# Optimization experiments

Measured on AMD Instinct MI355X. Metric: run time of the kernel, lower is better.

The kernel has to match this reference:

```python
import jax, jax.numpy as jnp
import numpy as np

VOCAB, EMB, UNITS = 2000, 64, 512
B, T = 64, 128

def lstm(x_emb, Wx, Wh, b, h0, c0):
    """Keras LSTM: gates order (i, f, g, o), sigmoid recurrent activation, tanh activation.
    x_emb: [B, T, EMB]. Returns (H [B,T,U], h [B,U], c [B,U])."""
    # Precompute input contribution for all timesteps (one big GEMM)
    xz = jnp.einsum('bte,eu->btu', x_emb, Wx) + b  # [B, T, 4U]

    def step(carry, xz_t):
        h, c = carry
        z = xz_t + h @ Wh  # [B, 4U]
        i, f, g, o = jnp.split(z, 4, axis=-1)
        i = jax.nn.sigmoid(i)
        f = jax.nn.sigmoid(f)
        g = jnp.tanh(g)
        o = jax.nn.sigmoid(o)
        c = f * c + i * g
        h = o * jnp.tanh(c)
        return (h, c), h

    (h, c), H = jax.lax.scan(step, (h0, c0), jnp.swapaxes(xz, 0, 1))
    return jnp.swapaxes(H, 0, 1), h, c


def setup_inputs() -> dict:
    key = jax.random.key(0)
    ks = jax.random.split(key, 10)
    s = 0.05
    return {
        'x': jax.random.randint(ks[0], (B, T), 0, VOCAB),
        'y': jax.random.randint(ks[1], (B, T), 0, VOCAB),
        'enc_emb': jax.random.normal(ks[2], (VOCAB, EMB), jnp.float32) * s,
        'enc_Wx': jax.random.normal(ks[3], (EMB, 4 * UNITS), jnp.float32) * s,
        'enc_Wh': jax.random.normal(ks[4], (UNITS, 4 * UNITS), jnp.float32) * s,
        'enc_b': jnp.zeros((4 * UNITS,), jnp.float32),
        'dec_emb': jax.random.normal(ks[5], (VOCAB, EMB), jnp.float32) * s,
        'dec_Wx': jax.random.normal(ks[6], (EMB, 4 * UNITS), jnp.float32) * s,
        'dec_Wh': jax.random.normal(ks[7], (UNITS, 4 * UNITS), jnp.float32) * s,
        'dec_b': jnp.zeros((4 * UNITS,), jnp.float32),
        'dense_W': jax.random.normal(ks[8], (2 * UNITS, VOCAB), jnp.float32) * s,
        'dense_b': jnp.zeros((VOCAB,), jnp.float32),
    }


def reference(x, y, enc_emb, enc_Wx, enc_Wh, enc_b,
              dec_emb, dec_Wx, dec_Wh, dec_b, dense_W, dense_b):
    z0 = jnp.zeros((x.shape[0], UNITS), jnp.float32)
    # Encoder
    H, h, c = lstm(enc_emb[x], enc_Wx, enc_Wh, enc_b, z0, z0)  # H: [B,T,U]
    # Decoder LSTM
    s0 = h
    S, h2, c2 = lstm(dec_emb[y], dec_Wx, dec_Wh, dec_b, h, c)  # S: [B,T,U]
    # Shifted states as attention queries (teacher forcing, Luong dot-attention)
    S_ = jnp.concatenate([s0[:, None, :], S[:, :-1, :]], axis=1)  # [B,T,U]
    scores = jnp.einsum('bqu,bku->bqk', S_, H)  # [B,T,T]
    A = jnp.einsum('bqk,bku->bqu', jax.nn.softmax(scores, axis=-1), H)
    yo = jnp.concatenate([S, A], axis=-1)  # [B,T,2U]
    return jax.nn.softmax(yo @ dense_W + dense_b, axis=-1)  # [B,T,VOCAB]
```

## Files before the change

### kernel.cpp

```cpp
#include <hip/hip_runtime.h>
#include <math.h>

#define NB 64
#define NT 128
#define NE 64
#define NU 512
#define NG 2048
#define NV 2000
#define BU (NB*NU)
#define GRID_LSTM 256
#define KTOT 576
#define HS 584
#define WSTRIDE 584
#define SMEM_BYTES (64*WSTRIDE*2 + 16*HS*2 + 2*8*64*4)

typedef __attribute__((ext_vector_type(8))) short bf16x8;
typedef __attribute__((ext_vector_type(4))) float f32x4;
typedef __attribute__((ext_vector_type(8))) unsigned short u16x8;

__device__ __forceinline__ unsigned short f2bf(float x) {
    unsigned int u = __float_as_uint(x);
    u += 0x7FFFu + ((u >> 16) & 1u);
    return (unsigned short)(u >> 16);
}
__device__ __forceinline__ float fsigmoid(float x) {
    return __builtin_amdgcn_rcpf(1.f + __expf(-x));
}
__device__ __forceinline__ float ftanh(float x) {
    return 1.f - 2.f * __builtin_amdgcn_rcpf(__expf(2.f * x) + 1.f);
}

__global__ __launch_bounds__(512, 1)
void lstm2_coop(const int* __restrict__ xids, const int* __restrict__ yids,
                const unsigned short* __restrict__ embb_e,
                const unsigned short* __restrict__ embb_d,
                const unsigned short* __restrict__ WhT_e,
                const unsigned short* __restrict__ WhT_d,
                const float* __restrict__ enc_b, const float* __restrict__ dec_b,
                float* __restrict__ Hbuf, float* __restrict__ Sbuf,
                float* __restrict__ hping, float* __restrict__ hfin,
                unsigned int* __restrict__ flags)
{
    extern __shared__ char smem[];
    unsigned short* whb  = (unsigned short*)smem;
    unsigned short* hlds = (unsigned short*)(smem + 64 * WSTRIDE * 2);
    float* zbuf = (float*)(smem + 64 * WSTRIDE * 2 + 16 * HS * 2);

    const int tid  = threadIdx.x;
    const int wv   = tid >> 6;
    const int cl   = tid & 63;
    const int bk   = blockIdx.x;
    const int rg   = bk & 7;
    const int cgi  = bk >> 3;
    const int brow0 = rg * 8;
    const int u0    = cgi * 16;

    const int bl  = tid >> 4;
    const int uug = tid & 15;
    float creg = 0.f;
    float b4[4] = {0.f, 0.f, 0.f, 0.f};
    if (tid < 128) {
#pragma unroll
        for (int g = 0; g < 4; ++g) b4[g] = enc_b[g * 512 + u0 + uug];
    }

    {
        const int cp = tid >> 3, ch = tid & 7;
        const int cg = (cp >> 4) * 512 + u0 + (cp & 15);
        const uint4* src = reinterpret_cast<const uint4*>(WhT_e + (size_t)cg * KTOT + ch * 72);
        uint4* dst = reinterpret_cast<uint4*>(whb + cp * WSTRIDE + ch * 72);
#pragma unroll
        for (int i = 0; i < 9; ++i) dst[i] = src[i];
    }

    const int col = wv * 64 + cl;
#pragma unroll
    for (int b = 0; b < 8; ++b) hlds[b * HS + col] = 0;
    for (int i = tid; i < 8 * HS; i += 512) hlds[8 * HS + i] = 0;
    {
        const int idb = xids[(brow0 + wv) * NT + 0];
        hlds[wv * HS + 512 + cl] = embb_e[(size_t)idb * NE + cl];
    }
    unsigned int* fl = flags + rg * 64;

    for (int T = 0; T < 2 * NT; ++T) {
        const int t = T & (NT - 1);
        float* Ho = (T < NT) ? Hbuf : Sbuf;
        __syncthreads();

        {
            const int g = wv & 3, half = wv >> 2;
            const int rr = cl & 15, kh = cl >> 4;
            f32x4 acc = {0.f, 0.f, 0.f, 0.f};
            const unsigned short* arow = hlds + rr * HS;
            const unsigned short* brow = whb + (g * 16 + rr) * WSTRIDE;
#pragma unroll
            for (int kt = 0; kt < 9; ++kt) {
                const int kb = (half * 9 + kt) * 32 + kh * 8;
                bf16x8 af = *reinterpret_cast<const bf16x8*>(arow + kb);
                bf16x8 bf = *reinterpret_cast<const bf16x8*>(brow + kb);
                acc = __builtin_amdgcn_mfma_f32_16x16x32_bf16(af, bf, acc, 0, 0, 0);
            }
            if (cl < 32) {
#pragma unroll
                for (int reg = 0; reg < 4; ++reg)
                    zbuf[half * 512 + (kh * 4 + reg) * 64 + g * 16 + rr] = acc[reg];
            }
        }
        __syncthreads();

        float h_ = 0.f;
        if (tid < 128) {
            float z[4];
#pragma unroll
            for (int g = 0; g < 4; ++g)
                z[g] = b4[g] + zbuf[bl * 64 + g * 16 + uug]
                             + zbuf[512 + bl * 64 + g * 16 + uug];
            const float i_ = fsigmoid(z[0]);
            const float f_ = fsigmoid(z[1]);
            const float g_ = ftanh(z[2]);
            const float o_ = fsigmoid(z[3]);
            creg = f_ * creg + i_ * g_;
            h_ = o_ * ftanh(creg);
            float* hw = hping + ((T + 1) & 1) * BU;
            __hip_atomic_store(&hw[(brow0 + bl) * NU + u0 + uug], h_,
                               __ATOMIC_RELAXED, __HIP_MEMORY_SCOPE_AGENT);
        }
        if (T == 2 * NT - 1) {
            if (tid < 128)
                Ho[((size_t)(brow0 + bl) * NT + t) * NU + u0 + uug] = h_;
            break;
        }

        if (tid < 128)
            asm volatile("s_waitcnt vmcnt(0)" ::: "memory");
        __syncthreads();

        if (tid < 128 && (tid & 63) == 0)
            __hip_atomic_store(&fl[(tid >> 6) * 32 + cgi], (unsigned)(T + 1),
                               __ATOMIC_RELAXED, __HIP_MEMORY_SCOPE_AGENT);
        if (tid < 128) {
            Ho[((size_t)(brow0 + bl) * NT + t) * NU + u0 + uug] = h_;
            if (T == NT - 1)
                hfin[(brow0 + bl) * NU + u0 + uug] = h_;
        }

        {
            const int Tn = T + 1;
            const int* nids = (Tn < NT) ? xids : yids;
            const unsigned short* nemb = (Tn < NT) ? embb_e : embb_d;
            const int idb = nids[(brow0 + wv) * NT + (Tn & (NT - 1))];
            hlds[wv * HS + 512 + cl] = nemb[(size_t)idb * NE + cl];
        }

        if (wv == 0) {
            const unsigned target = (unsigned)(T + 1);
            while (true) {
                unsigned v = __hip_atomic_load(&fl[cl], __ATOMIC_RELAXED,
                                               __HIP_MEMORY_SCOPE_AGENT);
#pragma unroll
                for (int o = 16; o; o >>= 1) {
                    unsigned v2 = (unsigned)__shfl_xor((int)v, o);
                    v = v2 < v ? v2 : v;
                }
                if (v >= target) break;
                __builtin_amdgcn_s_sleep(1);
            }
        }
        __syncthreads();

        {
            const float* hr = hping + ((T + 1) & 1) * BU + (size_t)brow0 * NU;
            float tmp[8];
#pragma unroll
            for (int b = 0; b < 8; ++b)
                tmp[b] = __hip_atomic_load(const_cast<float*>(&hr[b * NU + col]),
                                           __ATOMIC_RELAXED, __HIP_MEMORY_SCOPE_AGENT);
#pragma unroll
            for (int b = 0; b < 8; ++b) hlds[b * HS + col] = f2bf(tmp[b]);
        }

        if (T == NT - 1) {
            const int cp = tid >> 3, ch = tid & 7;
            const int cg = (cp >> 4) * 512 + u0 + (cp & 15);
            const uint4* src = reinterpret_cast<const uint4*>(WhT_d + (size_t)cg * KTOT + ch * 72);
            uint4* dst = reinterpret_cast<uint4*>(whb + cp * WSTRIDE + ch * 72);
#pragma unroll
            for (int i = 0; i < 9; ++i) dst[i] = src[i];
            if (tid < 128) {
#pragma unroll
                for (int g = 0; g < 4; ++g) b4[g] = dec_b[g * 512 + u0 + uug];
            }
        }
    }
}

__global__ __launch_bounds__(256)
void conv_emb2(const float* __restrict__ e0, const float* __restrict__ e1,
               unsigned short* __restrict__ o0, unsigned short* __restrict__ o1,
               int n, int nbh)
{
    int b = blockIdx.x;
    const float* e = e0; unsigned short* o = o0;
    if (b >= nbh) { b -= nbh; e = e1; o = o1; }
    const int i = (b * 256 + threadIdx.x) * 8;
    if (i >= n) return;
    const float4 v0 = reinterpret_cast<const float4*>(e + i)[0];
    const float4 v1 = reinterpret_cast<const float4*>(e + i)[1];
    u16x8 r;
    r[0] = f2bf(v0.x); r[1] = f2bf(v0.y); r[2] = f2bf(v0.z); r[3] = f2bf(v0.w);
    r[4] = f2bf(v1.x); r[5] = f2bf(v1.y); r[6] = f2bf(v1.z); r[7] = f2bf(v1.w);
    *reinterpret_cast<u16x8*>(o + i) = r;
}

__global__ __launch_bounds__(256)
void conv_WhT2(const float* __restrict__ Wh_e, const float* __restrict__ Wx_e,
               const float* __restrict__ Wh_d, const float* __restrict__ Wx_d,
               unsigned short* __restrict__ WhT_e, unsigned short* __restrict__ WhT_d)
{
    __shared__ float lt[64][65];
    const float* Wh = (blockIdx.z == 0) ? Wh_e : Wh_d;
    const float* Wx = (blockIdx.z == 0) ? Wx_e : Wx_d;
    unsigned short* WhT = (blockIdx.z == 0) ? WhT_e : WhT_d;
    const int tid = threadIdx.x;
    const int c0 = blockIdx.x * 64;
    const int k0 = blockIdx.y * 64;
#pragma unroll
    for (int j = 0; j < 16; ++j) {
        const int lin = tid + 256 * j;
        const int kk = lin >> 6, cc = lin & 63;
        const int k = k0 + kk;
        lt[cc][kk] = (k < 512) ? Wh[(size_t)k * NG + c0 + cc]
                               : Wx[(size_t)(k - 512) * NG + c0 + cc];
    }
    __syncthreads();
    const int c = tid >> 2, kseg = tid & 3;
    unsigned short tmp[16];
#pragma unroll
    for (int m = 0; m < 16; ++m)
        tmp[m] = f2bf(lt[c][kseg * 16 + m]);
    unsigned short* dst = WhT + (size_t)(c0 + c) * KTOT + k0 + kseg * 16;
    *reinterpret_cast<u16x8*>(dst)     = *reinterpret_cast<u16x8*>(tmp);
    *reinterpret_cast<u16x8*>(dst + 8) = *reinterpret_cast<u16x8*>(tmp + 8);
}

__global__ __launch_bounds__(256)
void attn_kernel(const float* __restrict__ S, const float* __restrict__ Hbuf,
                 const float* __restrict__ s0, float* __restrict__ A)
{
    const int tid  = threadIdx.x;
    const int wv   = tid >> 6;
    const int lane = tid & 63;
    const int b    = blockIdx.x >> 5;
    const int q    = (blockIdx.x & 31) * 4 + wv;

    const float* qrow = (q == 0) ? (s0 + (size_t)b * NU)
                                 : (S + ((size_t)b * NT + (q - 1)) * NU);
    const float4* q4 = reinterpret_cast<const float4*>(qrow);
    const float4 qa = q4[lane], qb = q4[64 + lane];
    const float4* Hb = reinterpret_cast<const float4*>(Hbuf + (size_t)b * NT * NU);

    float sr0 = 0.f, sr1 = 0.f;
    for (int k = 0; k < NT; ++k) {
        const float4* hk = Hb + (size_t)k * 128;
        float4 ha = hk[lane], hc = hk[64 + lane];
        float d = qa.x * ha.x + qa.y * ha.y + qa.z * ha.z + qa.w * ha.w
                + qb.x * hc.x + qb.y * hc.y + qb.z * hc.z + qb.w * hc.w;
#pragma unroll
        for (int o = 32; o; o >>= 1) d += __shfl_xor(d, o);
        if ((k & 63) == lane) { if (k < 64) sr0 = d; else sr1 = d; }
        if ((k & 31) == 31) __syncthreads();
    }

    float m = fmaxf(sr0, sr1);
#pragma unroll
    for (int o = 32; o; o >>= 1) m = fmaxf(m, __shfl_xor(m, o));
    float e0 = expf(sr0 - m), e1 = expf(sr1 - m);
    float s = e0 + e1;
#pragma unroll
    for (int o = 32; o; o >>= 1) s += __shfl_xor(s, o);
    const float inv = 1.f / s;
    e0 *= inv; e1 *= inv;

    float4 acc0 = {0.f, 0.f, 0.f, 0.f}, acc1 = {0.f, 0.f, 0.f, 0.f};
    for (int k = 0; k < 64; ++k) {
        const float wk = __shfl(e0, k);
        const float4* hk = Hb + (size_t)k * 128;
        float4 ha = hk[lane], hc = hk[64 + lane];
        acc0.x += wk * ha.x; acc0.y += wk * ha.y; acc0.z += wk * ha.z; acc0.w += wk * ha.w;
        acc1.x += wk * hc.x; acc1.y += wk * hc.y; acc1.z += wk * hc.z; acc1.w += wk * hc.w;
        if ((k & 31) == 31) __syncthreads();
    }
    for (int k = 0; k < 64; ++k) {
        const float wk = __shfl(e1, k);
        const float4* hk = Hb + (size_t)(64 + k) * 128;
        float4 ha = hk[lane], hc = hk[64 + lane];
        acc0.x += wk * ha.x; acc0.y += wk * ha.y; acc0.z += wk * ha.z; acc0.w += wk * ha.w;
        acc1.x += wk * hc.x; acc1.y += wk * hc.y; acc1.z += wk * hc.z; acc1.w += wk * hc.w;
        if ((k & 31) == 31) __syncthreads();
    }
    float4* Aq = reinterpret_cast<float4*>(A + ((size_t)b * NT + q) * NU);
    Aq[lane] = acc0;
    Aq[64 + lane] = acc1;
}

__global__ __launch_bounds__(256)
void conv_Wt(const float* __restrict__ W, unsigned short* __restrict__ Wt)
{
    __shared__ float lt[64][65];
    const int tid = threadIdx.x;
    const int c0 = blockIdx.x * 64;
    const int k0 = blockIdx.y * 64;
#pragma unroll
    for (int j = 0; j < 16; ++j) {
        const int lin = tid + 256 * j;
        const int kk = lin >> 6, cc = lin & 63;
        const int c = c0 + cc;
        lt[cc][kk] = (c < NV) ? W[(size_t)(k0 + kk) * NV + c] : 0.f;
    }
    __syncthreads();
    const int c = tid >> 2, kseg = tid & 3;
    unsigned short tmp[16];
#pragma unroll
    for (int m = 0; m < 16; ++m)
        tmp[m] = f2bf(lt[c][kseg * 16 + m]);
    unsigned short* dst = Wt + (size_t)(c0 + c) * 1024 + k0 + kseg * 16;
    *reinterpret_cast<u16x8*>(dst)     = *reinterpret_cast<u16x8*>(tmp);
    *reinterpret_cast<u16x8*>(dst + 8) = *reinterpret_cast<u16x8*>(tmp + 8);
}

__global__ __launch_bounds__(256)
void dense_mfma(const float* __restrict__ S, const float* __restrict__ A,
                const unsigned short* __restrict__ Wt,
                const float* __restrict__ bias, float* __restrict__ out)
{
    __shared__ unsigned short Asm[128][40];
    __shared__ unsigned short Bsm[128][40];
    const int tid  = threadIdx.x;
    const int wave = tid >> 6, lane = tid & 63;
    const int wm = wave >> 1, wn = wave & 1;
    const int r0 = blockIdx.y * 128, c0 = blockIdx.x * 128;
    const int rr = lane & 15, kh = lane >> 4;

    f32x4 acc[4][4];
#pragma unroll
    for (int m = 0; m < 4; ++m)
#pragma unroll
        for (int n = 0; n < 4; ++n) acc[m][n] = (f32x4){0.f, 0.f, 0.f, 0.f};

    for (int k0 = 0; k0 < 1024; k0 += 32) {
        __syncthreads();
#pragma unroll
        for (int h = 0; h < 2; ++h) {
            const int row = (tid >> 2) + h * 64, seg = tid & 3;
            const int kc = k0 + seg * 8;
            const float* asrc = (kc < 512) ? (S + (size_t)(r0 + row) * NU + kc)
                                           : (A + (size_t)(r0 + row) * NU + (kc - 512));
            const float4 a0 = reinterpret_cast<const float4*>(asrc)[0];
            const float4 a1 = reinterpret_cast<const float4*>(asrc)[1];
            u16x8 av;
            av[0] = f2bf(a0.x); av[1] = f2bf(a0.y); av[2] = f2bf(a0.z); av[3] = f2bf(a0.w);
            av[4] = f2bf(a1.x); av[5] = f2bf(a1.y); av[6] = f2bf(a1.z); av[7] = f2bf(a1.w);
            *reinterpret_cast<u16x8*>(&Asm[row][seg * 8]) = av;
            *reinterpret_cast<uint4*>(&Bsm[row][seg * 8]) =
                *reinterpret_cast<const uint4*>(Wt + (size_t)(c0 + row) * 1024 + k0 + seg * 8);
        }
        __syncthreads();
        bf16x8 af[4], bfr[4];
#pragma unroll
        for (int m = 0; m < 4; ++m)
            af[m] = *reinterpret_cast<const bf16x8*>(&Asm[wm * 64 + m * 16 + rr][kh * 8]);
#pragma unroll
        for (int n = 0; n < 4; ++n)
            bfr[n] = *reinterpret_cast<const bf16x8*>(&Bsm[wn * 64 + n * 16 + rr][kh * 8]);
#pragma unroll
        for (int m = 0; m < 4; ++m)
#pragma unroll
            for (int n = 0; n < 4; ++n)
                acc[m][n] = __builtin_amdgcn_mfma_f32_16x16x32_bf16(af[m], bfr[n], acc[m][n], 0, 0, 0);
    }

#pragma unroll
    for (int m = 0; m < 4; ++m) {
#pragma unroll
        for (int n = 0; n < 4; ++n) {
            const int c = c0 + wn * 64 + n * 16 + rr;
            if (c < NV) {
                const float bc = bias[c];
#pragma unroll
                for (int reg = 0; reg < 4; ++reg) {
                    const int r = r0 + wm * 64 + m * 16 + kh * 4 + reg;
                    out[(size_t)r * NV + c] = acc[m][n][reg] + bc;
                }
            }
        }
    }
}

__global__ __launch_bounds__(256)
void softmax_rows(float* __restrict__ out)
{
    __shared__ float red[4];
    const int t = threadIdx.x;
    float* row = out + (size_t)blockIdx.x * NV;

    float v[8];
    float m = -INFINITY;
#pragma unroll
    for (int i = 0; i < 8; ++i) {
        const int j = t + 256 * i;
        v[i] = (j < NV) ? row[j] : -INFINITY;
        m = fmaxf(m, v[i]);
    }
#pragma unroll
    for (int o = 32; o; o >>= 1) m = fmaxf(m, __shfl_xor(m, o));
    if ((t & 63) == 0) red[t >> 6] = m;
    __syncthreads();
    m = fmaxf(fmaxf(red[0], red[1]), fmaxf(red[2], red[3]));
    __syncthreads();

    float s = 0.f;
#pragma unroll
    for (int i = 0; i < 8; ++i) {
        const int j = t + 256 * i;
        if (j < NV) { v[i] = expf(v[i] - m); s += v[i]; }
    }
#pragma unroll
    for (int o = 32; o; o >>= 1) s += __shfl_xor(s, o);
    if ((t & 63) == 0) red[t >> 6] = s;
    __syncthreads();
    const float inv = 1.f / (red[0] + red[1] + red[2] + red[3]);
#pragma unroll
    for (int i = 0; i < 8; ++i) {
        const int j = t + 256 * i;
        if (j < NV) row[j] = v[i] * inv;
    }
}

extern "C" void kernel_launch(void* const* d_in, const int* in_sizes, int n_in,
                              void* d_out, int out_size, void* d_ws, size_t ws_size,
                              hipStream_t stream)
{
    const int*   x       = (const int*)  d_in[0];
    const int*   y       = (const int*)  d_in[1];
    const float* enc_emb = (const float*)d_in[2];
    const float* enc_Wx  = (const float*)d_in[3];
    const float* enc_Wh  = (const float*)d_in[4];
    const float* enc_b   = (const float*)d_in[5];
    const float* dec_emb = (const float*)d_in[6];
    const float* dec_Wx  = (const float*)d_in[7];
    const float* dec_Wh  = (const float*)d_in[8];
    const float* dec_b   = (const float*)d_in[9];
    const float* dns_W   = (const float*)d_in[10];
    const float* dns_b   = (const float*)d_in[11];
    float* out = (float*)d_out;

    float* ws   = (float*)d_ws;
    float* Hbuf = ws;
    float* Sbuf = Hbuf + (size_t)NB * NT * NU;
    float* Abuf = Sbuf + (size_t)NB * NT * NU;
    unsigned short* Wt = (unsigned short*)(Abuf + (size_t)NB * NT * NU);
    float* hping = (float*)(Wt + (size_t)2048 * 1024);
    float* hfin  = hping + 2 * BU;
    unsigned int* bar0 = (unsigned int*)(hfin + BU);
    unsigned short* WhT_e = (unsigned short*)(bar0 + 512);
    unsigned short* WhT_d = WhT_e + (size_t)2048 * KTOT;
    unsigned short* embb_e = WhT_d + (size_t)2048 * KTOT;
    unsigned short* embb_d = embb_e + (size_t)NV * NE;

    hipMemsetAsync(bar0, 0, 512 * sizeof(unsigned int), stream);

    (void)hipFuncSetAttribute(reinterpret_cast<const void*>(lstm2_coop),
                              hipFuncAttributeMaxDynamicSharedMemorySize, SMEM_BYTES);

    const int nemb = NV * NE, nbh = (nemb / 8 + 255) / 256;
    conv_emb2<<<dim3(2 * nbh), dim3(256), 0, stream>>>(enc_emb, dec_emb, embb_e, embb_d, nemb, nbh);
    conv_WhT2<<<dim3(32, 9, 2), dim3(256), 0, stream>>>(enc_Wh, enc_Wx, dec_Wh, dec_Wx, WhT_e, WhT_d);
    conv_Wt<<<dim3(32, 16), dim3(256), 0, stream>>>(dns_W, Wt);

    {
        void* args[] = { (void*)&x, (void*)&y, (void*)&embb_e, (void*)&embb_d,
                         (void*)&WhT_e, (void*)&WhT_d, (void*)&enc_b, (void*)&dec_b,
                         (void*)&Hbuf, (void*)&Sbuf, (void*)&hping, (void*)&hfin,
                         (void*)&bar0 };
        (void)hipLaunchCooperativeKernel(reinterpret_cast<void*>(lstm2_coop),
                                         dim3(GRID_LSTM), dim3(512), args,
                                         SMEM_BYTES, stream);
    }
    attn_kernel<<<dim3(NB * 32), dim3(256), 0, stream>>>(Sbuf, Hbuf, hfin, Abuf);
    dense_mfma<<<dim3(16, 64), dim3(256), 0, stream>>>(Sbuf, Abuf, Wt, dns_b, out);
    softmax_rows<<<dim3(NB * NT), dim3(256), 0, stream>>>(out);
}
```

Before: 985.0 us.

## Rewrite attention with bf16 MFMA and feed dense GEMM a fused bf16 concat buffer

Result: faster. 880.7 us (-10.6%).

```diff
diff --git a/kernel.cpp b/kernel.cpp
--- a/kernel.cpp
+++ b/kernel.cpp
@@ -14,6 +14,14 @@
 #define WSTRIDE 584
 #define SMEM_BYTES (64*WSTRIDE*2 + 16*HS*2 + 2*8*64*4)
 
+#define ASSC 129
+#define APB  136
+#define OFF_SSC 0
+#define OFF_PB  66048
+#define OFF_ASM 100864
+#define OFF_BSM 111104
+#define SMEM_ATT 121344
+
 typedef __attribute__((ext_vector_type(8))) short bf16x8;
 typedef __attribute__((ext_vector_type(4))) float f32x4;
 typedef __attribute__((ext_vector_type(8))) unsigned short u16x8;
@@ -39,6 +47,7 @@
                 const float* __restrict__ enc_b, const float* __restrict__ dec_b,
                 float* __restrict__ Hbuf, float* __restrict__ Sbuf,
                 float* __restrict__ hping, float* __restrict__ hfin,
+                unsigned short* __restrict__ yo,
                 unsigned int* __restrict__ flags)
 {
     extern __shared__ char smem[];
@@ -127,8 +136,11 @@
                                __ATOMIC_RELAXED, __HIP_MEMORY_SCOPE_AGENT);
         }
         if (T == 2 * NT - 1) {
-            if (tid < 128)
-                Ho[((size_t)(brow0 + bl) * NT + t) * NU + u0 + uug] = h_;
+            if (tid < 128) {
+                const size_t r = (size_t)(brow0 + bl) * NT + t;
+                Ho[r * NU + u0 + uug] = h_;
+                yo[r * 1024 + u0 + uug] = f2bf(h_);
+            }
             break;
         }
 
@@ -140,7 +152,9 @@
             __hip_atomic_store(&fl[(tid >> 6) * 32 + cgi], (unsigned)(T + 1),
                                __ATOMIC_RELAXED, __HIP_MEMORY_SCOPE_AGENT);
         if (tid < 128) {
-            Ho[((size_t)(brow0 + bl) * NT + t) * NU + u0 + uug] = h_;
+            const size_t r = (size_t)(brow0 + bl) * NT + t;
+            Ho[r * NU + u0 + uug] = h_;
+            if (T >= NT) yo[r * 1024 + u0 + uug] = f2bf(h_);
             if (T == NT - 1)
                 hfin[(brow0 + bl) * NU + u0 + uug] = h_;
         }
@@ -192,6 +206,144 @@
                 for (int g = 0; g < 4; ++g) b4[g] = dec_b[g * 512 + u0 + uug];
             }
         }
+    }
+}
+
+__global__ __launch_bounds__(256)
+void attn_mfma(const float* __restrict__ S, const float* __restrict__ Hbuf,
+               const float* __restrict__ s0, unsigned short* __restrict__ yo)
+{
+    extern __shared__ char smem[];
+    float* Ssc = (float*)(smem + OFF_SSC);
+    unsigned short* Bc  = (unsigned short*)(smem + OFF_SSC);
+    unsigned short* Pb  = (unsigned short*)(smem + OFF_PB);
+    unsigned short* Asm_ = (unsigned short*)(smem + OFF_ASM);
+    unsigned short* Bsm_ = (unsigned short*)(smem + OFF_BSM);
+
+    const int tid  = threadIdx.x;
+    const int wave = tid >> 6, lane = tid & 63;
+    const int wm = wave >> 1, wn = wave & 1;
+    const int rr = lane & 15, kh = lane >> 4;
+    const int b = blockIdx.x;
+    const float* Hb = Hbuf + (size_t)b * NT * NU;
+
+    f32x4 acc[4][4];
+#pragma unroll
+    for (int m = 0; m < 4; ++m)
+#pragma unroll
+        for (int n = 0; n < 4; ++n) acc[m][n] = (f32x4){0.f, 0.f, 0.f, 0.f};
+
+    for (int k0 = 0; k0 < 512; k0 += 32) {
+        __syncthreads();
+#pragma unroll
+        for (int h = 0; h < 2; ++h) {
+            const int row = (tid >> 2) + h * 64, seg = tid & 3;
+            const float* qsrc = (row == 0) ? (s0 + (size_t)b * NU)
+                                           : (S + ((size_t)b * NT + row - 1) * NU);
+            const float4 a0 = reinterpret_cast<const float4*>(qsrc + k0 + seg * 8)[0];
+            const float4 a1 = reinterpret_cast<const float4*>(qsrc + k0 + seg * 8)[1];
+            u16x8 av;
+            av[0] = f2bf(a0.x); av[1] = f2bf(a0.y); av[2] = f2bf(a0.z); av[3] = f2bf(a0.w);
+            av[4] = f2bf(a1.x); av[5] = f2bf(a1.y); av[6] = f2bf(a1.z); av[7] = f2bf(a1.w);
+            *reinterpret_cast<u16x8*>(Asm_ + row * 40 + seg * 8) = av;
+            const float4 b0 = reinterpret_cast<const float4*>(Hb + (size_t)row * NU + k0 + seg * 8)[0];
+            const float4 b1 = reinterpret_cast<const float4*>(Hb + (size_t)row * NU + k0 + seg * 8)[1];
+            u16x8 bv;
+            bv[0] = f2bf(b0.x); bv[1] = f2bf(b0.y); bv[2] = f2bf(b0.z); bv[3] = f2bf(b0.w);
+            bv[4] = f2bf(b1.x); bv[5] = f2bf(b1.y); bv[6] = f2bf(b1.z); bv[7] = f2bf(b1.w);
+            *reinterpret_cast<u16x8*>(Bsm_ + row * 40 + seg * 8) = bv;
+        }
+        __syncthreads();
+        bf16x8 af[4], bfr[4];
+#pragma unroll
+        for (int m = 0; m < 4; ++m)
+            af[m] = *reinterpret_cast<const bf16x8*>(Asm_ + (wm * 64 + m * 16 + rr) * 40 + kh * 8);
+#pragma unroll
+        for (int n = 0; n < 4; ++n)
+            bfr[n] = *reinterpret_cast<const bf16x8*>(Bsm_ + (wn * 64 + n * 16 + rr) * 40 + kh * 8);
+#pragma unroll
+        for (int m = 0; m < 4; ++m)
+#pragma unroll
+            for (int n = 0; n < 4; ++n)
+                acc[m][n] = __builtin_amdgcn_mfma_f32_16x16x32_bf16(af[m], bfr[n], acc[m][n], 0, 0, 0);
+    }
+    __syncthreads();
+#pragma unroll
+    for (int m = 0; m < 4; ++m)
+#pragma unroll
+        for (int n = 0; n < 4; ++n)
+#pragma unroll
+            for (int reg = 0; reg < 4; ++reg)
+                Ssc[(wm * 64 + m * 16 + kh * 4 + reg) * ASSC + wn * 64 + n * 16 + rr] = acc[m][n][reg];
+    __syncthreads();
+
+    {
+        const int row = tid >> 1, half = tid & 1;
+        float* srow = Ssc + row * ASSC + half * 64;
+        float mx = -INFINITY;
+#pragma unroll 8
+        for (int j = 0; j < 64; ++j) mx = fmaxf(mx, srow[j]);
+        mx = fmaxf(mx, __shfl_xor(mx, 1));
+        float sum = 0.f;
+#pragma unroll 8
+        for (int j = 0; j < 64; ++j) { float e = __expf(srow[j] - mx); srow[j] = e; sum += e; }
+        sum += __shfl_xor(sum, 1);
+        const float inv = 1.f / sum;
+#pragma unroll 8
+        for (int j = 0; j < 64; ++j)
+            Pb[row * APB + half * 64 + j] = f2bf(srow[j] * inv);
+    }
+
+    for (int nc = 0; nc < 4; ++nc) {
+        const int uc0 = nc * 128;
+        __syncthreads();
+#pragma unroll
+        for (int c4 = 0; c4 < 4; ++c4) {
+            const int kk = (tid >> 3) + 32 * c4;
+            const int u0t = (tid & 7) * 16;
+            const float* hsrc = Hb + (size_t)kk * NU + uc0 + u0t;
+#pragma unroll
+            for (int q4 = 0; q4 < 4; ++q4) {
+                const float4 v = reinterpret_cast<const float4*>(hsrc)[q4];
+                Bc[(u0t + q4 * 4 + 0) * APB + kk] = f2bf(v.x);
+                Bc[(u0t + q4 * 4 + 1) * APB + kk] = f2bf(v.y);
+                Bc[(u0t + q4 * 4 + 2) * APB + kk] = f2bf(v.z);
+                Bc[(u0t + q4 * 4 + 3) * APB + kk] = f2bf(v.w);
+            }
+        }
+        __syncthreads();
+
+        f32x4 oacc[4][4];
+#pragma unroll
+        for (int m = 0; m < 4; ++m)
+#pragma unroll
+            for (int n = 0; n < 4; ++n) oacc[m][n] = (f32x4){0.f, 0.f, 0.f, 0.f};
+#pragma unroll
+        for (int ks = 0; ks < 4; ++ks) {
+            bf16x8 af[4], bfr[4];
+#pragma unroll
+            for (int m = 0; m < 4; ++m)
+                af[m] = *reinterpret_cast<const bf16x8*>(Pb + (wm * 64 + m * 16 + rr) * APB + ks * 32 + kh * 8);
+#pragma unroll
+            for (int n = 0; n < 4; ++n)
+                bfr[n] = *reinterpret_cast<const bf16x8*>(Bc + (wn * 64 + n * 16 + rr) * APB + ks * 32 + kh * 8);
+#pragma unroll
+            for (int m = 0; m < 4; ++m)
+#pragma unroll
+                for (int n = 0; n < 4; ++n)
+                    oacc[m][n] = __builtin_amdgcn_mfma_f32_16x16x32_bf16(af[m], bfr[n], oacc[m][n], 0, 0, 0);
+        }
+#pragma unroll
+        for (int m = 0; m < 4; ++m)
+#pragma unroll
+            for (int n = 0; n < 4; ++n) {
+                const int u = uc0 + wn * 64 + n * 16 + rr;
+#pragma unroll
+                for (int reg = 0; reg < 4; ++reg) {
+                    const int q = wm * 64 + m * 16 + kh * 4 + reg;
+                    yo[((size_t)b * NT + q) * 1024 + 512 + u] = f2bf(oacc[m][n][reg]);
+                }
+            }
     }
 }
 
@@ -245,66 +397,6 @@
 }
 
 __global__ __launch_bounds__(256)
-void attn_kernel(const float* __restrict__ S, const float* __restrict__ Hbuf,
-                 const float* __restrict__ s0, float* __restrict__ A)
-{
-    const int tid  = threadIdx.x;
-    const int wv   = tid >> 6;
-    const int lane = tid & 63;
-    const int b    = blockIdx.x >> 5;
-    const int q    = (blockIdx.x & 31) * 4 + wv;
-
-    const float* qrow = (q == 0) ? (s0 + (size_t)b * NU)
-                                 : (S + ((size_t)b * NT + (q - 1)) * NU);
-    const float4* q4 = reinterpret_cast<const float4*>(qrow);
-    const float4 qa = q4[lane], qb = q4[64 + lane];
-    const float4* Hb = reinterpret_cast<const float4*>(Hbuf + (size_t)b * NT * NU);
-
-    float sr0 = 0.f, sr1 = 0.f;
-    for (int k = 0; k < NT; ++k) {
-        const float4* hk = Hb + (size_t)k * 128;
-        float4 ha = hk[lane], hc = hk[64 + lane];
-        float d = qa.x * ha.x + qa.y * ha.y + qa.z * ha.z + qa.w * ha.w
-                + qb.x * hc.x + qb.y * hc.y + qb.z * hc.z + qb.w * hc.w;
-#pragma unroll
-        for (int o = 32; o; o >>= 1) d += __shfl_xor(d, o);
-        if ((k & 63) == lane) { if (k < 64) sr0 = d; else sr1 = d; }
-        if ((k & 31) == 31) __syncthreads();
-    }
-
-    float m = fmaxf(sr0, sr1);
-#pragma unroll
-    for (int o = 32; o; o >>= 1) m = fmaxf(m, __shfl_xor(m, o));
-    float e0 = expf(sr0 - m), e1 = expf(sr1 - m);
-    float s = e0 + e1;
-#pragma unroll
-    for (int o = 32; o; o >>= 1) s += __shfl_xor(s, o);
-    const float inv = 1.f / s;
-    e0 *= inv; e1 *= inv;
-
-    float4 acc0 = {0.f, 0.f, 0.f, 0.f}, acc1 = {0.f, 0.f, 0.f, 0.f};
-    for (int k = 0; k < 64; ++k) {
-        const float wk = __shfl(e0, k);
-        const float4* hk = Hb + (size_t)k * 128;
-        float4 ha = hk[lane], hc = hk[64 + lane];
-        acc0.x += wk * ha.x; acc0.y += wk * ha.y; acc0.z += wk * ha.z; acc0.w += wk * ha.w;
-        acc1.x += wk * hc.x; acc1.y += wk * hc.y; acc1.z += wk * hc.z; acc1.w += wk * hc.w;
-        if ((k & 31) == 31) __syncthreads();
-    }
-    for (int k = 0; k < 64; ++k) {
-        const float wk = __shfl(e1, k);
-        const float4* hk = Hb + (size_t)(64 + k) * 128;
-        float4 ha = hk[lane], hc = hk[64 + lane];
-        acc0.x += wk * ha.x; acc0.y += wk * ha.y; acc0.z += wk * ha.z; acc0.w += wk * ha.w;
-        acc1.x += wk * hc.x; acc1.y += wk * hc.y; acc1.z += wk * hc.z; acc1.w += wk * hc.w;
-        if ((k & 31) == 31) __syncthreads();
-    }
-    float4* Aq = reinterpret_cast<float4*>(A + ((size_t)b * NT + q) * NU);
-    Aq[lane] = acc0;
-    Aq[64 + lane] = acc1;
-}
-
-__global__ __launch_bounds__(256)
 void conv_Wt(const float* __restrict__ W, unsigned short* __restrict__ Wt)
 {
     __shared__ float lt[64][65];
@@ -330,7 +422,7 @@
 }
 
 __global__ __launch_bounds__(256)
-void dense_mfma(const float* __restrict__ S, const float* __restrict__ A,
+void dense_mfma(const unsigned short* __restrict__ yo,
                 const unsigned short* __restrict__ Wt,
                 const float* __restrict__ bias, float* __restrict__ out)
 {
@@ -353,15 +445,8 @@
 #pragma unroll
         for (int h = 0; h < 2; ++h) {
             const int row = (tid >> 2) + h * 64, seg = tid & 3;
-            const int kc = k0 + seg * 8;
-            const float* asrc = (kc < 512) ? (S + (size_t)(r0 + row) * NU + kc)
-                                           : (A + (size_t)(r0 + row) * NU + (kc - 512));
-            const float4 a0 = reinterpret_cast<const float4*>(asrc)[0];
-            const float4 a1 = reinterpret_cast<const float4*>(asrc)[1];
-            u16x8 av;
-            av[0] = f2bf(a0.x); av[1] = f2bf(a0.y); av[2] = f2bf(a0.z); av[3] = f2bf(a0.w);
-            av[4] = f2bf(a1.x); av[5] = f2bf(a1.y); av[6] = f2bf(a1.z); av[7] = f2bf(a1.w);
-            *reinterpret_cast<u16x8*>(&Asm[row][seg * 8]) = av;
+            *reinterpret_cast<uint4*>(&Asm[row][seg * 8]) =
+                *reinterpret_cast<const uint4*>(yo + (size_t)(r0 + row) * 1024 + k0 + seg * 8);
             *reinterpret_cast<uint4*>(&Bsm[row][seg * 8]) =
                 *reinterpret_cast<const uint4*>(Wt + (size_t)(c0 + row) * 1024 + k0 + seg * 8);
         }
@@ -458,8 +543,8 @@
     float* ws   = (float*)d_ws;
     float* Hbuf = ws;
     float* Sbuf = Hbuf + (size_t)NB * NT * NU;
-    float* Abuf = Sbuf + (size_t)NB * NT * NU;
-    unsigned short* Wt = (unsigned short*)(Abuf + (size_t)NB * NT * NU);
+    unsigned short* yo = (unsigned short*)(Sbuf + (size_t)NB * NT * NU);
+    unsigned short* Wt = yo + (size_t)NB * NT * 1024;
     float* hping = (float*)(Wt + (size_t)2048 * 1024);
     float* hfin  = hping + 2 * BU;
     unsigned int* bar0 = (unsigned int*)(hfin + BU);
@@ -472,6 +557,8 @@
 
     (void)hipFuncSetAttribute(reinterpret_cast<const void*>(lstm2_coop),
                               hipFuncAttributeMaxDynamicSharedMemorySize, SMEM_BYTES);
+    (void)hipFuncSetAttribute(reinterpret_cast<const void*>(attn_mfma),
+                              hipFuncAttributeMaxDynamicSharedMemorySize, SMEM_ATT);
 
     const int nemb = NV * NE, nbh = (nemb / 8 + 255) / 256;
     conv_emb2<<<dim3(2 * nbh), dim3(256), 0, stream>>>(enc_emb, dec_emb, embb_e, embb_d, nemb, nbh);
@@ -482,12 +569,12 @@
         void* args[] = { (void*)&x, (void*)&y, (void*)&embb_e, (void*)&embb_d,
                          (void*)&WhT_e, (void*)&WhT_d, (void*)&enc_b, (void*)&dec_b,
                          (void*)&Hbuf, (void*)&Sbuf, (void*)&hping, (void*)&hfin,
-                         (void*)&bar0 };
+                         (void*)&yo, (void*)&bar0 };
         (void)hipLaunchCooperativeKernel(reinterpret_cast<void*>(lstm2_coop),
                                          dim3(GRID_LSTM), dim3(512), args,
                                          SMEM_BYTES, stream);
     }
-    attn_kernel<<<dim3(NB * 32), dim3(256), 0, stream>>>(Sbuf, Hbuf, hfin, Abuf);
-    dense_mfma<<<dim3(16, 64), dim3(256), 0, stream>>>(Sbuf, Abuf, Wt, dns_b, out);
+    attn_mfma<<<dim3(NB), dim3(256), SMEM_ATT, stream>>>(Sbuf, Hbuf, hfin, yo);
+    dense_mfma<<<dim3(16, 64), dim3(256), 0, stream>>>(yo, Wt, dns_b, out);
     softmax_rows<<<dim3(NB * NT), dim3(256), 0, stream>>>(out);
 }
```
